# Performance work log

Hardware: AMD Instinct MI355X
Metric: run time of the kernel (lower is better)

## Reference

```python
import jax, jax.numpy as jnp
import numpy as np

D = 100  # embedding_dim (hard-coded in the original module)


def _prelu(x, a):
    return jnp.where(x >= 0, x, a * x)


def setup_inputs() -> dict:
    key = jax.random.key(0)
    ks = jax.random.split(key, 12)
    B, S, L, R, V = 32, 50, 20, 16, 50000
    T = L * R  # tokens per sentence = len_max_sentence * n_routes
    return {
        "stories": jax.random.randint(ks[0], (B, S, T), 0, V),
        "queries": jax.random.randint(ks[1], (B, L), 0, V),
        "emb": 0.1 * jax.random.normal(ks[2], (V, D), dtype=jnp.float32),
        "in_mult": jnp.ones((T, D), dtype=jnp.float32),
        "q_mult": jnp.ones((L, D), dtype=jnp.float32),
        "keys": 0.1 * jax.random.normal(ks[3], (R, D), dtype=jnp.float32),
        "init_state": 0.1 * jax.random.normal(ks[4], (D,), dtype=jnp.float32),
        "U": 0.1 * jax.random.normal(ks[5], (R * D, D), dtype=jnp.float32),
        "Vw": 0.1 * jax.random.normal(ks[6], (R * D, R * D), dtype=jnp.float32),
        "Ww": 0.1 * jax.random.normal(ks[7], (R * D, R * D), dtype=jnp.float32),
        "Hw": 0.1 * jax.random.normal(ks[8], (D, D), dtype=jnp.float32),
        "Rw": 0.1 * jax.random.normal(ks[9], (V, D), dtype=jnp.float32),
        "alpha_in": jnp.ones((1,), dtype=jnp.float32),  # PReLU(init=1)
        "alpha_q": jnp.ones((1,), dtype=jnp.float32),
    }


def reference(stories, queries, emb, in_mult, q_mult, keys, init_state,
              U, Vw, Ww, Hw, Rw, alpha_in, alpha_q):
    B, S, T = stories.shape
    R = keys.shape[0]
    emb0 = emb.at[0].set(0.0)  # padding_idx=0 row is zero
    # stories -> [B,S,T,D] -> route-sum -> [B,S,R,D]
    x = emb0[stories] * in_mult
    x = x.reshape(B, S, R, T // R, D).sum(axis=3)
    # V(keys.flatten()) is constant across timesteps
    v_keys = (keys.reshape(-1) @ Vw.T).reshape(R, D)
    state0 = jnp.tile(init_state[None, None, :], (B, 1, 1))  # [B,1,D]

    def step(state, sent):  # state [B,1,D], sent [B,R,D]
        gate = jax.nn.sigmoid(sent * state + sent * keys)
        u = (state.reshape(B, D) @ U.T).reshape(B, R, D)
        w = (sent.reshape(B, R * D) @ Ww.T).reshape(B, R, D)
        cand = _prelu(u + v_keys + w, alpha_in)
        # null-sentence mask: zero out positions where gate == sigmoid(0) = 0.5
        mask = jax.lax.stop_gradient(jnp.where(gate == 0.5, 0.0, 1.0))
        state = state + (cand * gate * mask).sum(axis=1, keepdims=True)
        # torch.norm over singleton dim=1 (= elementwise abs), kept faithful
        state = state / jnp.sqrt(jnp.sum(state * state, axis=1, keepdims=True))
        return state, None

    state, _ = jax.lax.scan(step, state0, jnp.swapaxes(x, 0, 1))

    q = (emb0[queries] * q_mult).sum(axis=1, keepdims=True)  # [B,1,D]
    h = _prelu(q + (state.reshape(B, D) @ Hw.T).reshape(B, 1, D), alpha_q)
    return h.reshape(B, D) @ Rw.T  # [B, vocab]
```

## Files before the change

### kernel.cpp

```cpp
#include <hip/hip_runtime.h>
#include <cstddef>
#include <cstdint>

#define B_  32
#define S_  50
#define L_  20
#define R_  16
#define D_  100
#define V_  50000
#define T_  320
#define RD_ 1600
#define BS_ 1600
#define NG_ 25
#define NP_ 16

typedef float v4f __attribute__((ext_vector_type(4)));
typedef unsigned short u16;
#define NTL(p)  __builtin_nontemporal_load((const v4f*)(p))

__device__ __forceinline__ float uf(unsigned u) { return __uint_as_float(u); }

__device__ __forceinline__ void bsplit(float a, unsigned& h, unsigned& l) {
  const unsigned bits = __float_as_uint(a);
  const unsigned hb = bits & 0xffff0000u;
  h = hb >> 16;
  l = __float_as_uint(a - __uint_as_float(hb)) >> 16;
}

__device__ __forceinline__ void bsplit4(float4 a, uint2& h, uint2& l) {
  unsigned h0,h1,h2,h3,l0,l1,l2,l3;
  bsplit(a.x, h0, l0); bsplit(a.y, h1, l1);
  bsplit(a.z, h2, l2); bsplit(a.w, h3, l3);
  h.x = h0 | (h1 << 16); h.y = h2 | (h3 << 16);
  l.x = l0 | (l1 << 16); l.y = l2 | (l3 << 16);
}

__global__ __launch_bounds__(512) void setup_kernel(
    const int* __restrict__ stories, const float* __restrict__ emb,
    const float* __restrict__ in_mult, const float* __restrict__ U,
    const float* __restrict__ Vw, const float* __restrict__ keys,
    const float* __restrict__ init_state, const float* __restrict__ Ww,
    float* __restrict__ x,
    u16* __restrict__ wh, u16* __restrict__ wl,
    float* __restrict__ table, float* __restrict__ vk, float* __restrict__ u0)
{
  const int blk = blockIdx.x, tid = threadIdx.x;
  if (blk < 1600) {
    __shared__ int toks[T_];
    const int* st = stories + (size_t)blk * T_;
    if (tid < T_) toks[tid] = st[tid];
    __syncthreads();
    if (tid < 400) {
      const int j4 = tid * 4;
      const int r  = j4 / D_;
      const int d4 = j4 - r * D_;
      float4 acc = make_float4(0.f, 0.f, 0.f, 0.f);
      #pragma unroll
      for (int l = 0; l < 20; ++l) {
        const int t = r * 20 + l;
        const int tok = toks[t];
        if (tok != 0) {
          float4 e = *(const float4*)&emb[(size_t)tok * D_ + d4];
          float4 m = *(const float4*)&in_mult[(size_t)t * D_ + d4];
          acc.x += e.x * m.x; acc.y += e.y * m.y;
          acc.z += e.z * m.z; acc.w += e.w * m.w;
        }
      }
      *(float4*)&x[(size_t)blk * RD_ + j4] = acc;
    }
  } else if (blk < 2000) {
    const int q = blk - 1600;
    const int g = q >> 4, p = q & 15;
    const float s0 = (p & 1) ? -1.f : 1.f;
    const float s1 = (p & 2) ? -1.f : 1.f;
    const float s2 = (p & 4) ? -1.f : 1.f;
    const float s3 = (p & 8) ? -1.f : 1.f;
    if (tid < 400) {
      const int j4 = tid * 4;
      float t[4];
      #pragma unroll
      for (int jj = 0; jj < 4; ++jj) {
        const float* ur = &U[(size_t)(j4 + jj) * D_ + 4 * g];
        t[jj] = s0*ur[0] + s1*ur[1] + s2*ur[2] + s3*ur[3];
      }
      *(float4*)&table[((size_t)(g * NP_ + p)) * RD_ + j4] =
          make_float4(t[0], t[1], t[2], t[3]);
    }
  } else if (blk < 2200) {
    const int wave = tid >> 6, lane = tid & 63;
    const int j = (blk - 2000) * 8 + wave;
    float acc = 0.f;
    for (int k = lane; k < RD_; k += 64)
      acc += keys[k] * Vw[(size_t)j * RD_ + k];
    #pragma unroll
    for (int off = 32; off > 0; off >>= 1) acc += __shfl_down(acc, off);
    if (lane == 0) vk[j] = acc;
  } else if (blk < 2400) {
    const int wave = tid >> 6, lane = tid & 63;
    const int j = (blk - 2200) * 8 + wave;
    const float* Ur = U + (size_t)j * D_;
    float acc = Ur[lane] * init_state[lane];
    if (lane < 36) acc += Ur[64 + lane] * init_state[64 + lane];
    #pragma unroll
    for (int off = 32; off > 0; off >>= 1) acc += __shfl_down(acc, off);
    if (lane == 0) u0[j] = acc;
  } else {
    const int e = ((blk - 2400) * 512 + tid) * 8;
    float4 a0 = *(const float4*)&Ww[e];
    float4 a1 = *(const float4*)&Ww[e + 4];
    uint2 h0, l0, h1, l1;
    bsplit4(a0, h0, l0);
    bsplit4(a1, h1, l1);
    uint4 hv = make_uint4(h0.x, h0.y, h1.x, h1.y);
    uint4 lv = make_uint4(l0.x, l0.y, l1.x, l1.y);
    *(uint4*)&wh[e] = hv;
    *(uint4*)&wl[e] = lv;
  }
}

typedef const __attribute__((address_space(1))) unsigned GAu;
typedef __attribute__((address_space(3))) unsigned LDSu;
#define GLL(SRC, DST) __builtin_amdgcn_global_load_lds((GAu*)(SRC), (LDSu*)(DST), 16, 0, 0)

__device__ __forceinline__ void mfma16(v4f& d, v4f a, v4f b) {
  asm("v_mfma_f32_16x16x32_bf16 %0, %1, %2, %0" : "+v"(d) : "v"(a), "v"(b));
}

__global__ __launch_bounds__(512) void gemm_mfma_kernel(
    const float* __restrict__ A,
    const u16* __restrict__ wh, const u16* __restrict__ wl,
    float* __restrict__ C)
{
  __shared__ __align__(16) char smem[2][4][8192];
  const int tid = threadIdx.x;
  const int lane = tid & 63, wid = tid >> 6;
  const int bm = blockIdx.y * 128, bn = blockIdx.x * 128;

  const int brow = wid * 16 + (lane >> 2);
  const int bkb  = (lane & 3) * 16;
  int rb = bn + brow; if (rb > 1599) rb = 1599;
  const int srcB = rb * 3200 + bkb;
  const int ldsB = wid * 1024;
  const char* gwh = (const char*)wh;
  const char* gwl = (const char*)wl;

  int arow[2], awofs[2];
  const int akseg = tid & 7;
  #pragma unroll
  for (int i = 0; i < 2; ++i) {
    const int r = i * 64 + (tid >> 3);
    int ra = bm + r; if (ra > 1599) ra = 1599;
    arow[i] = ra;
    awofs[i] = r * 64 + akseg * 8;
  }

  const int wm = wid >> 2, wn = wid & 3;
  const int r15 = lane & 15, q = lane >> 4;
  const int aoff = (wm * 64 + r15) * 64 + q * 16;
  const int boff = (wn * 32 + r15) * 64 + q * 16;

  v4f acc[4][2];
  #pragma unroll
  for (int i = 0; i < 4; ++i)
    #pragma unroll
    for (int j = 0; j < 2; ++j) acc[i][j] = (v4f)(0.f);

  auto stageB = [&](int buf, int kt) {
    const int kb = kt * 64;
    GLL(gwh + srcB + kb, &smem[buf][2][ldsB]);
    GLL(gwl + srcB + kb, &smem[buf][3][ldsB]);
  };

  float4 a4[2];

  #pragma unroll
  for (int i = 0; i < 2; ++i)
    a4[i] = *(const float4*)&A[(size_t)arow[i] * RD_ + akseg * 4];
  stageB(0, 0);
  #pragma unroll
  for (int i = 0; i < 2; ++i) {
    uint2 h, l; bsplit4(a4[i], h, l);
    *(uint2*)&smem[0][0][awofs[i]] = h;
    *(uint2*)&smem[0][1][awofs[i]] = l;
  }
  __syncthreads();

  for (int kt = 0; kt < 50; ++kt) {
    const int cur = kt & 1;
    if (kt < 49) {
      stageB(cur ^ 1, kt + 1);
      #pragma unroll
      for (int i = 0; i < 2; ++i)
        a4[i] = *(const float4*)&A[(size_t)arow[i] * RD_ + (kt + 1) * 32 + akseg * 4];
    }
    const char* s0 = &smem[cur][0][0];
    v4f ah[4], al[4], bh[2], bl[2];
    #pragma unroll
    for (int t = 0; t < 4; ++t) {
      ah[t] = *(const v4f*)(s0 +         aoff + t * 1024);
      al[t] = *(const v4f*)(s0 +  8192 + aoff + t * 1024);
    }
    #pragma unroll
    for (int t = 0; t < 2; ++t) {
      bh[t] = *(const v4f*)(s0 + 16384 + boff + t * 1024);
      bl[t] = *(const v4f*)(s0 + 24576 + boff + t * 1024);
    }
    #pragma unroll
    for (int im = 0; im < 4; ++im)
      #pragma unroll
      for (int in = 0; in < 2; ++in) {
        mfma16(acc[im][in], ah[im], bh[in]);
        mfma16(acc[im][in], ah[im], bl[in]);
        mfma16(acc[im][in], al[im], bh[in]);
      }
    if (kt < 49) {
      const int nxt = cur ^ 1;
      #pragma unroll
      for (int i = 0; i < 2; ++i) {
        uint2 h, l; bsplit4(a4[i], h, l);
        *(uint2*)&smem[nxt][0][awofs[i]] = h;
        *(uint2*)&smem[nxt][1][awofs[i]] = l;
      }
    }
    __syncthreads();
  }

  const int mb  = bm + wm * 64 + q * 4;
  const int nbq = bn + wn * 32 + r15;
  #pragma unroll
  for (int im = 0; im < 4; ++im) {
    #pragma unroll
    for (int in = 0; in < 2; ++in) {
      const int n = nbq + in * 16;
      const int m0 = mb + im * 16;
      if (n < 1600) {
        #pragma unroll
        for (int r = 0; r < 4; ++r)
          if (m0 + r < 1600)
            C[(size_t)(m0 + r) * RD_ + n] = acc[im][in][r];
      }
    }
  }
}

__global__ __launch_bounds__(512, 2) void scan_kernel(
    const float* __restrict__ x,
    const float* __restrict__ Wall,
    const float* __restrict__ table,
    const float* __restrict__ u0,
    const float* __restrict__ vkeys,
    const float* __restrict__ keys,
    const float* __restrict__ init_state,
    const float* __restrict__ alpha_in_p,
    const int*   __restrict__ queries,
    const float* __restrict__ emb,
    const float* __restrict__ q_mult,
    const float* __restrict__ Hw,
    const float* __restrict__ alpha_q_p,
    float* __restrict__ h_g)
{
  const int b = blockIdx.x, tid = threadIdx.x;
  __shared__ __align__(16) float s_state[D_];
  __shared__ __align__(16) float s_c[RD_];
  __shared__ float s_hw[D_ * 101];
  __shared__ unsigned long long s_mask[2];
  const float alpha = alpha_in_p[0];
  const bool active = (tid < 400);
  const int j4 = tid * 4;
  const int d4 = (j4 % D_);
  float4 kk = make_float4(0.f,0.f,0.f,0.f), vv = kk;
  const float* xb = x    + (size_t)b * S_ * RD_;
  const float* wb = Wall + (size_t)b * S_ * RD_;
  v4f bx[5], bw[5];
  #pragma unroll
  for (int i = 0; i < 5; ++i) { bx[i] = (v4f)(0.f); bw[i] = (v4f)(0.f); }
  if (active) {
    kk = *(const float4*)&keys[j4];
    vv = *(const float4*)&vkeys[j4];
    #pragma unroll
    for (int i = 0; i < 5; ++i) {
      bx[i] = NTL(&xb[(size_t)i * RD_ + j4]);
      bw[i] = NTL(&wb[(size_t)i * RD_ + j4]);
    }
  }
  if (tid < D_) s_state[tid] = init_state[tid];
  __syncthreads();

  for (int sg = 0; sg < S_; sg += 5) {
    #pragma unroll
    for (int i = 0; i < 5; ++i) {
      const int s = sg + i;
      if (active) {
        const v4f sent = bx[i], w = bw[i];
        const bool first = (s == 0);
        v4f tv[NG_];
        if (first) {
          tv[0] = *(const v4f*)&u0[j4];
        } else {
          const unsigned long long m0 = s_mask[0];
          const unsigned long long m1 = s_mask[1];
          #pragma unroll
          for (int g = 0; g < NG_; ++g) {
            const unsigned idx = (g < 16)
                ? (unsigned)((m0 >> (4 * g)) & 15ull)
                : (unsigned)((m1 >> (4 * g - 64)) & 15ull);
            tv[g] = *(const v4f*)&table[((size_t)(g * NP_) + idx) * RD_ + j4];
          }
        }
        __builtin_amdgcn_sched_barrier(0);
        if (s + 5 < S_) {
          bx[i] = NTL(&xb[(size_t)(s + 5) * RD_ + j4]);
          bw[i] = NTL(&wb[(size_t)(s + 5) * RD_ + j4]);
        }
        float4 sd = *(const float4*)&s_state[d4];
        float zx = sent.x * sd.x + sent.x * kk.x;
        float zy = sent.y * sd.y + sent.y * kk.y;
        float zz = sent.z * sd.z + sent.z * kk.z;
        float zw = sent.w * sd.w + sent.w * kk.w;
        float gx = 1.0f / (1.0f + expf(-zx));
        float gy = 1.0f / (1.0f + expf(-zy));
        float gz = 1.0f / (1.0f + expf(-zz));
        float gw = 1.0f / (1.0f + expf(-zw));
        v4f u = tv[0];
        if (!first) {
          #pragma unroll
          for (int g = 1; g < NG_; ++g) {
            u.x += tv[g].x; u.y += tv[g].y; u.z += tv[g].z; u.w += tv[g].w;
          }
        }
        float cx = u.x + vv.x + w.x; cx = cx >= 0.f ? cx : alpha * cx;
        float cy = u.y + vv.y + w.y; cy = cy >= 0.f ? cy : alpha * cy;
        float cz = u.z + vv.z + w.z; cz = cz >= 0.f ? cz : alpha * cz;
        float cw = u.w + vv.w + w.w; cw = cw >= 0.f ? cw : alpha * cw;
        v4f cc;
        cc.x = (gx == 0.5f) ? 0.f : cx * gx;
        cc.y = (gy == 0.5f) ? 0.f : cy * gy;
        cc.z = (gz == 0.5f) ? 0.f : cz * gz;
        cc.w = (gw == 0.5f) ? 0.f : cw * gw;
        *(v4f*)&s_c[j4] = cc;
      }
      __syncthreads();
      if (tid < D_) {
        float csum = 0.f;
        #pragma unroll
        for (int r = 0; r < R_; ++r) csum += s_c[r * D_ + tid];
        float v = s_state[tid] + csum;
        v = v / sqrtf(v * v);
        s_state[tid] = v;
        unsigned long long mask = __ballot(v < 0.f);
        if ((tid & 63) == 0) s_mask[tid >> 6] = mask;
      }
      __syncthreads();
    }
  }

  for (int f = tid; f < D_ * D_; f += 512) {
    const int row = f / D_, col = f - row * D_;
    s_hw[row * 101 + col] = Hw[f];
  }
  __syncthreads();
  if (tid < D_) {
    float q = 0.f;
    #pragma unroll
    for (int l = 0; l < L_; ++l) {
      const int tok = queries[b * L_ + l];
      if (tok != 0) q += emb[(size_t)tok * D_ + tid] * q_mult[l * D_ + tid];
    }
    float a = 0.f;
    #pragma unroll 4
    for (int k = 0; k < D_; ++k) a += s_state[k] * s_hw[tid * 101 + k];
    float h = q + a;
    const float aq = alpha_q_p[0];
    h = h >= 0.f ? h : aq * h;
    h_g[(size_t)b * D_ + tid] = h;
  }
}

__global__ __launch_bounds__(256) void out_kernel(
    const float* __restrict__ h_g, const float* __restrict__ Rw, float* __restrict__ out)
{
  __shared__ __align__(16) float sh[B_ * D_];
  __shared__ __align__(16) float sr[32 * D_];
  int tid = threadIdx.x;
  int v0 = blockIdx.x * 32;
  for (int i = tid; i < B_ * D_; i += 256) sh[i] = h_g[i];
  int nrows = V_ - v0; if (nrows > 32) nrows = 32;
  for (int i = tid; i < nrows * D_; i += 256) sr[i] = Rw[(size_t)v0 * D_ + i];
  __syncthreads();
  const float4* sh4 = (const float4*)sh;
  const float4* sr4 = (const float4*)sr;
  int tv = (tid & 15) * 2;
  int tb = (tid >> 4) * 2;
  float a00 = 0.f, a01 = 0.f, a10 = 0.f, a11 = 0.f;
  #pragma unroll
  for (int kc = 0; kc < 25; ++kc) {
    float4 h0 = sh4[tb * 25 + kc];
    float4 h1 = sh4[(tb + 1) * 25 + kc];
    float4 r0 = sr4[tv * 25 + kc];
    float4 r1 = sr4[(tv + 1) * 25 + kc];
    a00 += h0.x*r0.x + h0.y*r0.y + h0.z*r0.z + h0.w*r0.w;
    a01 += h0.x*r1.x + h0.y*r1.y + h0.z*r1.z + h0.w*r1.w;
    a10 += h1.x*r0.x + h1.y*r0.y + h1.z*r0.z + h1.w*r0.w;
    a11 += h1.x*r1.x + h1.y*r1.y + h1.z*r1.z + h1.w*r1.w;
  }
  if (tv < nrows) {
    out[(size_t)tb * V_ + v0 + tv] = a00;
    out[(size_t)(tb + 1) * V_ + v0 + tv] = a10;
  }
  if (tv + 1 < nrows) {
    out[(size_t)tb * V_ + v0 + tv + 1] = a01;
    out[(size_t)(tb + 1) * V_ + v0 + tv + 1] = a11;
  }
}

extern "C" void kernel_launch(void* const* d_in, const int* in_sizes, int n_in,
                              void* d_out, int out_size, void* d_ws, size_t ws_size,
                              hipStream_t stream) {
  const int*   stories    = (const int*)  d_in[0];
  const int*   queries    = (const int*)  d_in[1];
  const float* emb        = (const float*)d_in[2];
  const float* in_mult    = (const float*)d_in[3];
  const float* q_mult     = (const float*)d_in[4];
  const float* keys       = (const float*)d_in[5];
  const float* init_state = (const float*)d_in[6];
  const float* U          = (const float*)d_in[7];
  const float* Vw         = (const float*)d_in[8];
  const float* Ww         = (const float*)d_in[9];
  const float* Hw         = (const float*)d_in[10];
  const float* Rw         = (const float*)d_in[11];
  const float* alpha_in   = (const float*)d_in[12];
  const float* alpha_q    = (const float*)d_in[13];
  float* out = (float*)d_out;

  char* ws = (char*)d_ws;
  float* x     = (float*)(ws);
  float* Wall  = (float*)(ws + 10240000);
  float* table = (float*)(ws + 20480000);
  u16*   wwh   = (u16*)  (ws + 23040000);
  u16*   wwl   = (u16*)  (ws + 28160000);
  float* vk    = (float*)(ws + 33280000);
  float* u0    = (float*)(ws + 33286400);
  float* hbuf  = (float*)(ws + 33292800);

  setup_kernel<<<3025, 512, 0, stream>>>(stories, emb, in_mult, U, Vw, keys,
                                         init_state, Ww, x, wwh, wwl,
                                         table, vk, u0);
  gemm_mfma_kernel<<<dim3(13, 13), 512, 0, stream>>>(x, wwh, wwl, Wall);
  scan_kernel<<<B_, 512, 0, stream>>>(x, Wall, table, u0, vk, keys, init_state,
                                      alpha_in, queries, emb, q_mult, Hw, alpha_q,
                                      hbuf);
  out_kernel<<<(V_ + 31) / 32, 256, 0, stream>>>(hbuf, Rw, out);
}
```

Baseline: 363.0 us.

## Permute route-major layout so scan reduces per-dim via shuffles, one barrier per step

Rows of Ww, Vw and U, along with the table and vk/u0 outputs, are permuted so each group of 4 threads owns all 16 routes of one embedding dim. The scan kernel can then reduce the route sum with two xor shuffles and keep the state in registers. This drops the LDS s_c buffer, the second barrier and the serial 16-way reduction each step. Sign bits go into a double-buffered byte array and are decoded with a multiply trick. The costs are uncoalesced scalar loads of x and a block shrunk to 448 threads.

```diff
diff --git a/kernel.cpp b/kernel.cpp
--- a/kernel.cpp
+++ b/kernel.cpp
@@ -16,9 +16,8 @@
 
 typedef float v4f __attribute__((ext_vector_type(4)));
 typedef unsigned short u16;
-#define NTL(p)  __builtin_nontemporal_load((const v4f*)(p))
-
-__device__ __forceinline__ float uf(unsigned u) { return __uint_as_float(u); }
+#define NTL(p)   __builtin_nontemporal_load((const v4f*)(p))
+#define NTLS(p)  __builtin_nontemporal_load((const float*)(p))
 
 __device__ __forceinline__ void bsplit(float a, unsigned& h, unsigned& l) {
   const unsigned bits = __float_as_uint(a);
@@ -69,52 +68,60 @@
       *(float4*)&x[(size_t)blk * RD_ + j4] = acc;
     }
   } else if (blk < 2000) {
-    const int q = blk - 1600;
-    const int g = q >> 4, p = q & 15;
+    const int qq = blk - 1600;
+    const int g = qq >> 4, p = qq & 15;
     const float s0 = (p & 1) ? -1.f : 1.f;
     const float s1 = (p & 2) ? -1.f : 1.f;
     const float s2 = (p & 4) ? -1.f : 1.f;
     const float s3 = (p & 8) ? -1.f : 1.f;
     if (tid < 400) {
-      const int j4 = tid * 4;
+      const int d  = tid >> 2;
+      const int r0 = (tid & 3) * 4;
       float t[4];
       #pragma unroll
-      for (int jj = 0; jj < 4; ++jj) {
-        const float* ur = &U[(size_t)(j4 + jj) * D_ + 4 * g];
-        t[jj] = s0*ur[0] + s1*ur[1] + s2*ur[2] + s3*ur[3];
-      }
-      *(float4*)&table[((size_t)(g * NP_ + p)) * RD_ + j4] =
+      for (int ri = 0; ri < 4; ++ri) {
+        const int orig = (r0 + ri) * D_ + d;
+        const float* ur = &U[(size_t)orig * D_ + 4 * g];
+        t[ri] = s0*ur[0] + s1*ur[1] + s2*ur[2] + s3*ur[3];
+      }
+      *(float4*)&table[((size_t)(g * NP_ + p)) * RD_ + tid * 4] =
           make_float4(t[0], t[1], t[2], t[3]);
     }
   } else if (blk < 2200) {
     const int wave = tid >> 6, lane = tid & 63;
-    const int j = (blk - 2000) * 8 + wave;
+    const int jp = (blk - 2000) * 8 + wave;
+    const int orig = (jp & 15) * D_ + (jp >> 4);
     float acc = 0.f;
     for (int k = lane; k < RD_; k += 64)
-      acc += keys[k] * Vw[(size_t)j * RD_ + k];
+      acc += keys[k] * Vw[(size_t)orig * RD_ + k];
     #pragma unroll
     for (int off = 32; off > 0; off >>= 1) acc += __shfl_down(acc, off);
-    if (lane == 0) vk[j] = acc;
+    if (lane == 0) vk[jp] = acc;
   } else if (blk < 2400) {
     const int wave = tid >> 6, lane = tid & 63;
-    const int j = (blk - 2200) * 8 + wave;
-    const float* Ur = U + (size_t)j * D_;
+    const int jp = (blk - 2200) * 8 + wave;
+    const int orig = (jp & 15) * D_ + (jp >> 4);
+    const float* Ur = U + (size_t)orig * D_;
     float acc = Ur[lane] * init_state[lane];
     if (lane < 36) acc += Ur[64 + lane] * init_state[64 + lane];
     #pragma unroll
     for (int off = 32; off > 0; off >>= 1) acc += __shfl_down(acc, off);
-    if (lane == 0) u0[j] = acc;
+    if (lane == 0) u0[jp] = acc;
   } else {
-    const int e = ((blk - 2400) * 512 + tid) * 8;
-    float4 a0 = *(const float4*)&Ww[e];
-    float4 a1 = *(const float4*)&Ww[e + 4];
+    const int g   = (blk - 2400) * 512 + tid;
+    const int row = g / 200;
+    const int c8  = (g - row * 200) * 8;
+    const int orig = (row & 15) * D_ + (row >> 4);
+    const float* src = &Ww[(size_t)orig * RD_ + c8];
+    float4 a0 = *(const float4*)src;
+    float4 a1 = *(const float4*)(src + 4);
     uint2 h0, l0, h1, l1;
     bsplit4(a0, h0, l0);
     bsplit4(a1, h1, l1);
     uint4 hv = make_uint4(h0.x, h0.y, h1.x, h1.y);
     uint4 lv = make_uint4(l0.x, l0.y, l1.x, l1.y);
-    *(uint4*)&wh[e] = hv;
-    *(uint4*)&wl[e] = lv;
+    *(uint4*)&wh[(size_t)row * RD_ + c8] = hv;
+    *(uint4*)&wl[(size_t)row * RD_ + c8] = lv;
   }
 }
 
@@ -172,7 +179,6 @@
   };
 
   float4 a4[2];
-
   #pragma unroll
   for (int i = 0; i < 2; ++i)
     a4[i] = *(const float4*)&A[(size_t)arow[i] * RD_ + akseg * 4];
@@ -243,7 +249,7 @@
   }
 }
 
-__global__ __launch_bounds__(512, 2) void scan_kernel(
+__global__ __launch_bounds__(448, 2) void scan_kernel(
     const float* __restrict__ x,
     const float* __restrict__ Wall,
     const float* __restrict__ table,
@@ -261,29 +267,40 @@
 {
   const int b = blockIdx.x, tid = threadIdx.x;
   __shared__ __align__(16) float s_state[D_];
-  __shared__ __align__(16) float s_c[RD_];
   __shared__ float s_hw[D_ * 101];
-  __shared__ unsigned long long s_mask[2];
+  __shared__ __align__(16) unsigned char s_sign[2][112];
   const float alpha = alpha_in_p[0];
   const bool active = (tid < 400);
-  const int j4 = tid * 4;
-  const int d4 = (j4 % D_);
-  float4 kk = make_float4(0.f,0.f,0.f,0.f), vv = kk;
+  const int q4 = tid * 4;
+  const int d  = tid >> 2;
+  const int r0 = (tid & 3) * 4;
+  int xo0 = 0, xo1 = 0, xo2 = 0, xo3 = 0;
+  float kk0 = 0.f, kk1 = 0.f, kk2 = 0.f, kk3 = 0.f;
+  float4 vv = make_float4(0.f, 0.f, 0.f, 0.f);
+  float state_reg = 0.f;
   const float* xb = x    + (size_t)b * S_ * RD_;
   const float* wb = Wall + (size_t)b * S_ * RD_;
-  v4f bx[5], bw[5];
-  #pragma unroll
-  for (int i = 0; i < 5; ++i) { bx[i] = (v4f)(0.f); bw[i] = (v4f)(0.f); }
+  float4 bx[5], bw[5];
+  #pragma unroll
+  for (int i = 0; i < 5; ++i) {
+    bx[i] = make_float4(0.f, 0.f, 0.f, 0.f);
+    bw[i] = make_float4(0.f, 0.f, 0.f, 0.f);
+  }
   if (active) {
-    kk = *(const float4*)&keys[j4];
-    vv = *(const float4*)&vkeys[j4];
+    xo0 = (r0 + 0) * D_ + d;  xo1 = (r0 + 1) * D_ + d;
+    xo2 = (r0 + 2) * D_ + d;  xo3 = (r0 + 3) * D_ + d;
+    kk0 = keys[xo0]; kk1 = keys[xo1]; kk2 = keys[xo2]; kk3 = keys[xo3];
+    vv = *(const float4*)&vkeys[q4];
+    state_reg = init_state[d];
     #pragma unroll
     for (int i = 0; i < 5; ++i) {
-      bx[i] = NTL(&xb[(size_t)i * RD_ + j4]);
-      bw[i] = NTL(&wb[(size_t)i * RD_ + j4]);
-    }
-  }
-  if (tid < D_) s_state[tid] = init_state[tid];
+      const float* xr = xb + (size_t)i * RD_;
+      bx[i].x = NTLS(xr + xo0); bx[i].y = NTLS(xr + xo1);
+      bx[i].z = NTLS(xr + xo2); bx[i].w = NTLS(xr + xo3);
+      v4f wv = NTL(&wb[(size_t)i * RD_ + q4]);
+      bw[i] = make_float4(wv.x, wv.y, wv.z, wv.w);
+    }
+  }
   __syncthreads();
 
   for (int sg = 0; sg < S_; sg += 5) {
@@ -291,32 +308,40 @@
     for (int i = 0; i < 5; ++i) {
       const int s = sg + i;
       if (active) {
-        const v4f sent = bx[i], w = bw[i];
+        const float4 sent = bx[i], w = bw[i];
         const bool first = (s == 0);
         v4f tv[NG_];
         if (first) {
-          tv[0] = *(const v4f*)&u0[j4];
+          tv[0] = *(const v4f*)&u0[q4];
         } else {
-          const unsigned long long m0 = s_mask[0];
-          const unsigned long long m1 = s_mask[1];
+          const uint4* sp = (const uint4*)s_sign[s & 1];
+          unsigned wd[25];
+          uint4 s0v = sp[0]; wd[0]=s0v.x;  wd[1]=s0v.y;  wd[2]=s0v.z;  wd[3]=s0v.w;
+          uint4 s1v = sp[1]; wd[4]=s1v.x;  wd[5]=s1v.y;  wd[6]=s1v.z;  wd[7]=s1v.w;
+          uint4 s2v = sp[2]; wd[8]=s2v.x;  wd[9]=s2v.y;  wd[10]=s2v.z; wd[11]=s2v.w;
+          uint4 s3v = sp[3]; wd[12]=s3v.x; wd[13]=s3v.y; wd[14]=s3v.z; wd[15]=s3v.w;
+          uint4 s4v = sp[4]; wd[16]=s4v.x; wd[17]=s4v.y; wd[18]=s4v.z; wd[19]=s4v.w;
+          uint4 s5v = sp[5]; wd[20]=s5v.x; wd[21]=s5v.y; wd[22]=s5v.z; wd[23]=s5v.w;
+          uint4 s6v = sp[6]; wd[24]=s6v.x;
           #pragma unroll
           for (int g = 0; g < NG_; ++g) {
-            const unsigned idx = (g < 16)
-                ? (unsigned)((m0 >> (4 * g)) & 15ull)
-                : (unsigned)((m1 >> (4 * g - 64)) & 15ull);
-            tv[g] = *(const v4f*)&table[((size_t)(g * NP_) + idx) * RD_ + j4];
+            const unsigned idx = (wd[g] * 0x01020408u) >> 24;
+            tv[g] = *(const v4f*)&table[((size_t)(g * NP_) + idx) * RD_ + q4];
           }
         }
         __builtin_amdgcn_sched_barrier(0);
         if (s + 5 < S_) {
-          bx[i] = NTL(&xb[(size_t)(s + 5) * RD_ + j4]);
-          bw[i] = NTL(&wb[(size_t)(s + 5) * RD_ + j4]);
+          const float* xr = xb + (size_t)(s + 5) * RD_;
+          bx[i].x = NTLS(xr + xo0); bx[i].y = NTLS(xr + xo1);
+          bx[i].z = NTLS(xr + xo2); bx[i].w = NTLS(xr + xo3);
+          v4f wv = NTL(&wb[(size_t)(s + 5) * RD_ + q4]);
+          bw[i] = make_float4(wv.x, wv.y, wv.z, wv.w);
         }
-        float4 sd = *(const float4*)&s_state[d4];
-        float zx = sent.x * sd.x + sent.x * kk.x;
-        float zy = sent.y * sd.y + sent.y * kk.y;
-        float zz = sent.z * sd.z + sent.z * kk.z;
-        float zw = sent.w * sd.w + sent.w * kk.w;
+        const float sd = state_reg;
+        float zx = sent.x * sd + sent.x * kk0;
+        float zy = sent.y * sd + sent.y * kk1;
+        float zz = sent.z * sd + sent.z * kk2;
+        float zw = sent.w * sd + sent.w * kk3;
         float gx = 1.0f / (1.0f + expf(-zx));
         float gy = 1.0f / (1.0f + expf(-zy));
         float gz = 1.0f / (1.0f + expf(-zz));
@@ -332,29 +357,24 @@
         float cy = u.y + vv.y + w.y; cy = cy >= 0.f ? cy : alpha * cy;
         float cz = u.z + vv.z + w.z; cz = cz >= 0.f ? cz : alpha * cz;
         float cw = u.w + vv.w + w.w; cw = cw >= 0.f ? cw : alpha * cw;
-        v4f cc;
-        cc.x = (gx == 0.5f) ? 0.f : cx * gx;
-        cc.y = (gy == 0.5f) ? 0.f : cy * gy;
-        cc.z = (gz == 0.5f) ? 0.f : cz * gz;
-        cc.w = (gw == 0.5f) ? 0.f : cw * gw;
-        *(v4f*)&s_c[j4] = cc;
+        float p  = ((gx == 0.5f) ? 0.f : cx * gx)
+                 + ((gy == 0.5f) ? 0.f : cy * gy)
+                 + ((gz == 0.5f) ? 0.f : cz * gz)
+                 + ((gw == 0.5f) ? 0.f : cw * gw);
+        p += __shfl_xor(p, 1);
+        p += __shfl_xor(p, 2);
+        float v = state_reg + p;
+        state_reg = v / sqrtf(v * v);
+        if ((tid & 3) == 0) s_sign[(s + 1) & 1][d] = (v < 0.f) ? 1 : 0;
       }
       __syncthreads();
-      if (tid < D_) {
-        float csum = 0.f;
-        #pragma unroll
-        for (int r = 0; r < R_; ++r) csum += s_c[r * D_ + tid];
-        float v = s_state[tid] + csum;
-        v = v / sqrtf(v * v);
-        s_state[tid] = v;
-        unsigned long long mask = __ballot(v < 0.f);
-        if ((tid & 63) == 0) s_mask[tid >> 6] = mask;
-      }
-      __syncthreads();
-    }
-  }
-
-  for (int f = tid; f < D_ * D_; f += 512) {
+    }
+  }
+
+  if (active && (tid & 3) == 0) s_state[d] = state_reg;
+  __syncthreads();
+
+  for (int f = tid; f < D_ * D_; f += 448) {
     const int row = f / D_, col = f - row * D_;
     s_hw[row * 101 + col] = Hw[f];
   }
@@ -446,7 +466,7 @@
                                          init_state, Ww, x, wwh, wwl,
                                          table, vk, u0);
   gemm_mfma_kernel<<<dim3(13, 13), 512, 0, stream>>>(x, wwh, wwl, Wall);
-  scan_kernel<<<B_, 512, 0, stream>>>(x, Wall, table, u0, vk, keys, init_state,
+  scan_kernel<<<B_, 448, 0, stream>>>(x, Wall, table, u0, vk, keys, init_state,
                                       alpha_in, queries, emb, q_mult, Hw, alpha_q,
                                       hbuf);
   out_kernel<<<(V_ + 31) / 32, 256, 0, stream>>>(hbuf, Rw, out);
```

After: 372.2 us. 2.5% more time.
